# Optimization experiments

Measured on AMD Instinct MI355X. Metric: run time of the kernel, lower is better.

Reference implementation:

```python
import jax, jax.numpy as jnp
import numpy as np

B, N_HEADS, DIM, Z, X = 128, 12, 768, 7, 14


def _rpe_index(z, x):
    """2D concatenated self-attention relative positional encoding index.
    Tokens = z*z template tokens followed by x*x search tokens. Two token
    pairs share a bias index iff they have the same (dh, dw, region_i, region_j).
    """
    zh, zw = np.meshgrid(np.arange(z), np.arange(z), indexing='ij')
    xh, xw = np.meshgrid(np.arange(x), np.arange(x), indexing='ij')
    h = np.concatenate([zh.ravel(), xh.ravel()])
    w = np.concatenate([zw.ravel(), xw.ravel()])
    region = np.concatenate([np.zeros(z * z, np.int64), np.ones(x * x, np.int64)])
    dh = h[:, None] - h[None, :]
    dw = w[:, None] - w[None, :]
    rb = np.broadcast_to(region[:, None], dh.shape)
    rc = np.broadcast_to(region[None, :], dh.shape)
    key = np.stack([dh, dw, rb, rc], axis=-1).reshape(-1, 4)
    _, inv = np.unique(key, axis=0, return_inverse=True)
    return inv.reshape(dh.shape)  # (N, N) int


def setup_inputs() -> dict:
    key = jax.random.key(0)
    ks = jax.random.split(key, 4)
    N = Z * Z + X * X  # 245
    idx = _rpe_index(Z, X)
    n_bias = int(idx.max()) + 1
    return {
        "x": jax.random.normal(ks[0], (B, N, DIM), jnp.float32),
        "qkv_w": jax.random.normal(ks[1], (3 * DIM, DIM), jnp.float32) * 0.02,
        "proj_w": jax.random.normal(ks[2], (DIM, DIM), jnp.float32) * 0.02,
        "proj_b": jnp.zeros((DIM,), jnp.float32),
        "bias_table": jax.random.normal(ks[3], (N_HEADS, n_bias), jnp.float32) * 0.02,
        "rel_index": jnp.asarray(idx, jnp.int32),
    }


def reference(x, qkv_w, proj_w, proj_b, bias_table, rel_index):
    Bq, N, C = x.shape
    H = N_HEADS
    Dh = C // H
    scale = Dh ** -0.5
    # qkv projection (no bias): (B, N, 3, H, Dh)
    qkv = (x @ qkv_w.T).reshape(Bq, N, 3, H, Dh)
    q = jnp.moveaxis(qkv[:, :, 0], 2, 1)  # (B, H, N, Dh)
    k = jnp.moveaxis(qkv[:, :, 1], 2, 1)
    v = jnp.moveaxis(qkv[:, :, 2], 2, 1)
    attn = jnp.einsum('bhnd,bhmd->bhnm', q, k) * scale  # (B, H, N, N)
    # relative position bias gather: (H, N, N) broadcast over batch
    attn = attn + bias_table[:, rel_index][None]
    attn = jax.nn.softmax(attn, axis=-1)
    out = jnp.einsum('bhnm,bhmd->bhnd', attn, v)  # (B, H, N, Dh)
    out = jnp.moveaxis(out, 1, 2).reshape(Bq, N, C)
    return out @ proj_w.T + proj_b
```

## Files before the change

### kernel.cpp

```cpp
#include <hip/hip_runtime.h>
#include <hip/hip_bf16.h>
#include <stdint.h>
#include <math.h>

#define BATCH 128
#define NTOK 245
#define HEADS 12
#define DHEAD 64
#define CDIM 768
#define KT 24
#define SUBT 512
#define SCL 0.18033688f
#define PCLAMP 43.3f

typedef __attribute__((ext_vector_type(8))) short short8;
typedef __attribute__((ext_vector_type(4))) float f32x4;

__device__ __forceinline__ float bf2f(uint32_t hbits) {
    union { uint32_t u; float f; } v; v.u = hbits << 16; return v.f;
}
__device__ __forceinline__ uint32_t f2bf(float f) {
    union { float f; uint32_t u; } v; v.f = f;
    return (v.u + 0x7fffu + ((v.u >> 16) & 1u)) >> 16;
}
__device__ __forceinline__ ushort2 pk2bf(float x, float y) {
    union { __hip_bfloat162 h; ushort2 u; } c;
    c.h = __float22bfloat162_rn(make_float2(x, y));
    return c.u;
}
__device__ __forceinline__ size_t tiled_addr(int m, int k) {
    return (((size_t)(m >> 4) * KT + (k >> 5)) * 64 + ((k >> 3) & 3) * 16 + (m & 15)) * 8
           + (k & 7);
}
__device__ __forceinline__ void gl_lds16(const uint16_t* g, ushort* lds) {
    __builtin_amdgcn_global_load_lds(
        (const __attribute__((address_space(1))) void*)g,
        (__attribute__((address_space(3))) void*)lds,
        16, 0, 0);
}

#define N8_X  3010560
#define N8_WQ  221184
#define N8_WP   73728
__global__ __launch_bounds__(256)
void cvt_all(const float* __restrict__ x, const float* __restrict__ wq,
             const float* __restrict__ wp, uint16_t* __restrict__ xd,
             uint16_t* __restrict__ wqd, uint16_t* __restrict__ wpd)
{
    int i = blockIdx.x * 256 + threadIdx.x;
    const int stride = gridDim.x * 256;
    const int total = N8_X + N8_WQ + N8_WP;
    for (; i < total; i += stride) {
        const float* src; uint16_t* dst; int j;
        if (i < N8_X)              { src = x;  dst = xd;  j = i; }
        else if (i < N8_X + N8_WQ) { src = wq; dst = wqd; j = i - N8_X; }
        else                       { src = wp; dst = wpd; j = i - N8_X - N8_WQ; }
        const int sl = j & 63;
        const int tile = j >> 6;
        const int rt = tile / KT, kt = tile - rt * KT;
        const size_t soff = (size_t)(rt * 16 + (sl & 15)) * CDIM + kt * 32 + (sl >> 4) * 8;
        float4 a = *(const float4*)(src + soff);
        float4 b = *(const float4*)(src + soff + 4);
        ushort2 p0 = pk2bf(a.x, a.y), p1 = pk2bf(a.z, a.w);
        ushort2 p2 = pk2bf(b.x, b.y), p3 = pk2bf(b.z, b.w);
        uint4 o;
        o.x = (uint32_t)p0.x | ((uint32_t)p0.y << 16);
        o.y = (uint32_t)p1.x | ((uint32_t)p1.y << 16);
        o.z = (uint32_t)p2.x | ((uint32_t)p2.y << 16);
        o.w = (uint32_t)p3.x | ((uint32_t)p3.y << 16);
        *(uint4*)(dst + (size_t)j * 8) = o;
    }
}

__global__ __launch_bounds__(256)
void bias_pre(const float* __restrict__ bias_table, const int* __restrict__ rel,
              int n_bias, uint16_t* __restrict__ bias_t)
{
    const int h = blockIdx.x, j = blockIdx.y, q = threadIdx.x;
    float v = -43281.f;
    if (j < NTOK && q < NTOK)
        v = bias_table[(size_t)h * n_bias + rel[q * NTOK + j]] * 1.44269504f;
    bias_t[((size_t)h * 256 + j) * 256 + q] = (uint16_t)f2bf(v);
}

#define GEMM_LOOP                                                                \
    gl_lds16(gA0, &Af[0][w  ][0][0]);                                            \
    gl_lds16(gA1, &Af[0][w+4][0][0]);                                            \
    gl_lds16(gB0, &Bf[0][w  ][0][0]);                                            \
    gl_lds16(gB1, &Bf[0][w+4][0][0]);                                            \
    gl_lds16(gA0 + SUBT, &Af[1][w  ][0][0]);                                     \
    gl_lds16(gA1 + SUBT, &Af[1][w+4][0][0]);                                     \
    gl_lds16(gB0 + SUBT, &Bf[1][w  ][0][0]);                                     \
    gl_lds16(gB1 + SUBT, &Bf[1][w+4][0][0]);                                     \
    int cur = 0, nxt = 2;                                                        \
    _Pragma("unroll 1")                                                          \
    for (int t = 0; t < KT; ++t) {                                               \
        if (t == KT - 1) { asm volatile("s_waitcnt vmcnt(0) lgkmcnt(0)" ::: "memory"); } \
        else             { asm volatile("s_waitcnt vmcnt(4) lgkmcnt(0)" ::: "memory"); } \
        __builtin_amdgcn_s_barrier();                                            \
        if (t + 2 < KT) {                                                        \
            const int ko = (t + 2) * SUBT;                                       \
            gl_lds16(gA0 + ko, &Af[nxt][w  ][0][0]);                             \
            gl_lds16(gA1 + ko, &Af[nxt][w+4][0][0]);                             \
            gl_lds16(gB0 + ko, &Bf[nxt][w  ][0][0]);                             \
            gl_lds16(gB1 + ko, &Bf[nxt][w+4][0][0]);                             \
        }                                                                        \
        short8 af[4], bf[4];                                                     \
        _Pragma("unroll")                                                        \
        for (int m = 0; m < 4; ++m)                                              \
            af[m] = *(const short8*)&Af[cur][wr*4 + m][l][0];                    \
        _Pragma("unroll")                                                        \
        for (int n = 0; n < 4; ++n)                                              \
            bf[n] = *(const short8*)&Bf[cur][wc*4 + n][l][0];                    \
        _Pragma("unroll")                                                        \
        for (int m = 0; m < 4; ++m)                                              \
            _Pragma("unroll")                                                    \
            for (int n = 0; n < 4; ++n)                                          \
                acc[m][n] = __builtin_amdgcn_mfma_f32_16x16x32_bf16(bf[n], af[m], acc[m][n], 0, 0, 0); \
        cur = (cur == 2) ? 0 : cur + 1;                                          \
        nxt = (nxt == 2) ? 0 : nxt + 1;                                          \
    }

__global__ __launch_bounds__(256)
void qkv_gemm_mfma(const uint16_t* __restrict__ xb, const uint16_t* __restrict__ wq,
                   uint16_t* __restrict__ qkv)
{
    __shared__ ushort Af[3][8][64][8];
    __shared__ ushort Bf[3][8][64][8];
    const int t = threadIdx.x;
    const int w = t >> 6, l = t & 63;
    const int wr = w >> 1, wc = w & 1;
    const int lm = l & 15, lk = l >> 4;

    const int bid = blockIdx.x;
    const int xcd = bid & 7;
    const int wg = (xcd < 2 ? xcd * 552 : 1104 + (xcd - 2) * 551) + (bid >> 3);
    const int mtile = wg / 18, ctile = wg - mtile * 18;
    const int m0 = mtile * 128, c0 = ctile * 128;

    const uint16_t* gA0 = xb + ((size_t)(mtile*8 + w    ) * KT * 64 + l) * 8;
    const uint16_t* gA1 = xb + ((size_t)(mtile*8 + w + 4) * KT * 64 + l) * 8;
    const uint16_t* gB0 = wq + ((size_t)(ctile*8 + w    ) * KT * 64 + l) * 8;
    const uint16_t* gB1 = wq + ((size_t)(ctile*8 + w + 4) * KT * 64 + l) * 8;

    f32x4 acc[4][4];
    #pragma unroll
    for (int m = 0; m < 4; ++m)
        #pragma unroll
        for (int n = 0; n < 4; ++n) acc[m][n] = (f32x4){0.f,0.f,0.f,0.f};

    GEMM_LOOP

    int sArr[4], hArr[4], dArr[4];
    #pragma unroll
    for (int n = 0; n < 4; ++n) {
        int c = c0 + wc*64 + n*16 + lk*4;
        int s = c / CDIM; int rem = c - s * CDIM;
        sArr[n] = s; hArr[n] = rem >> 6; dArr[n] = rem & 63;
    }
    #pragma unroll
    for (int m = 0; m < 4; ++m) {
        int gm  = m0 + wr*64 + m*16 + lm;
        int b   = gm / NTOK;
        int tok = gm - b * NTOK;
        #pragma unroll
        for (int n = 0; n < 4; ++n) {
            ushort2 u0 = pk2bf(acc[m][n][0], acc[m][n][1]);
            ushort2 u1 = pk2bf(acc[m][n][2], acc[m][n][3]);
            uint2 pk;
            pk.x = (uint32_t)u0.x | ((uint32_t)u0.y << 16);
            pk.y = (uint32_t)u1.x | ((uint32_t)u1.y << 16);
            size_t addr = ((((size_t)b*3 + sArr[n])*HEADS + hArr[n])*NTOK + tok)*DHEAD + dArr[n];
            *(uint2*)(qkv + addr) = pk;
        }
    }
}

__global__ __launch_bounds__(512)
void attn_mfma(const uint16_t* __restrict__ qkv, const uint16_t* __restrict__ bias_t,
               uint16_t* __restrict__ o_t)
{
    __shared__ ushort Ks[256][72];
    __shared__ ushort Vt[64][264];
    __shared__ ushort Ps[8][16][72];
    const int bh = blockIdx.x;
    const int b = bh / HEADS, h = bh % HEADS;
    const int t = threadIdx.x;
    const int w = t >> 6, l = t & 63;
    const int lm = l & 15, lk = l >> 4;
    const int wq0 = w * 32;

    const uint16_t* qbase = qkv + (((size_t)b*3 + 0)*HEADS + h) * (NTOK*DHEAD);
    const uint16_t* kbase = qkv + (((size_t)b*3 + 1)*HEADS + h) * (NTOK*DHEAD);
    const uint16_t* vbase = qkv + (((size_t)b*3 + 2)*HEADS + h) * (NTOK*DHEAD);
    const uint16_t* btab  = bias_t + (size_t)h * 256 * 256;

    {
        const int col = (t & 7) * 8;
        #pragma unroll
        for (int p = 0; p < 4; ++p) {
            int row = p * 64 + (t >> 3);
            uint4 val = make_uint4(0u,0u,0u,0u);
            if (row < NTOK) val = *(const uint4*)(kbase + (size_t)row * DHEAD + col);
            *(uint4*)&Ks[row][col] = val;
        }
    }
    {
        const int j  = t >> 1;
        const int dh = (t & 1) * 32;
        uint4 r0 = make_uint4(0,0,0,0), r1 = r0, r2 = r0, r3 = r0;
        if (j < NTOK) {
            const uint16_t* src = vbase + (size_t)j * DHEAD + dh;
            r0 = *(const uint4*)(src);
            r1 = *(const uint4*)(src + 8);
            r2 = *(const uint4*)(src + 16);
            r3 = *(const uint4*)(src + 24);
        }
        union { uint4 v[4]; ushort s[32]; } u;
        u.v[0] = r0; u.v[1] = r1; u.v[2] = r2; u.v[3] = r3;
        #pragma unroll
        for (int i = 0; i < 32; ++i)
            Vt[dh + i][j] = u.s[i];
    }

    short8 qf[2][2];
    #pragma unroll
    for (int m = 0; m < 2; ++m) {
        int qrow = wq0 + m*16 + lm; if (qrow > NTOK-1) qrow = NTOK-1;
        #pragma unroll
        for (int k2 = 0; k2 < 2; ++k2)
            qf[m][k2] = *(const short8*)(qbase + (size_t)qrow * DHEAD + k2*32 + lk*8);
    }

    f32x4 acc_o[2][4];
    float lsum[2][4];
    #pragma unroll
    for (int m = 0; m < 2; ++m) {
        #pragma unroll
        for (int n = 0; n < 4; ++n) acc_o[m][n] = (f32x4){0.f,0.f,0.f,0.f};
        #pragma unroll
        for (int r = 0; r < 4; ++r) lsum[m][r] = 0.f;
    }

    __syncthreads();

    for (int jb = 0; jb < 4; ++jb) {
        short8 kf[4][2], vf[4][2];
        #pragma unroll
        for (int n = 0; n < 4; ++n)
            #pragma unroll
            for (int k2 = 0; k2 < 2; ++k2) {
                kf[n][k2] = *(const short8*)&Ks[jb*64 + n*16 + lm][k2*32 + lk*8];
                vf[n][k2] = *(const short8*)&Vt[n*16 + lm][jb*64 + k2*32 + lk*8];
            }

        #pragma unroll
        for (int m = 0; m < 2; ++m) {
            f32x4 sv[4];
            __builtin_amdgcn_s_setprio(1);
            #pragma unroll
            for (int n = 0; n < 4; ++n) {
                f32x4 z = (f32x4){0.f,0.f,0.f,0.f};
                sv[n] = __builtin_amdgcn_mfma_f32_16x16x32_bf16(qf[m][0], kf[n][0], z, 0, 0, 0);
                sv[n] = __builtin_amdgcn_mfma_f32_16x16x32_bf16(qf[m][1], kf[n][1], sv[n], 0, 0, 0);
            }
            __builtin_amdgcn_s_setprio(0);
            #pragma unroll
            for (int n = 0; n < 4; ++n) {
                uint2 bb = *(const uint2*)(btab + (size_t)(jb*64 + n*16 + lm) * 256 + wq0 + m*16 + lk*4);
                float s0 = fmaf(sv[n][0], SCL, bf2f(bb.x & 0xffffu));
                float s1 = fmaf(sv[n][1], SCL, bf2f(bb.x >> 16));
                float s2 = fmaf(sv[n][2], SCL, bf2f(bb.y & 0xffffu));
                float s3 = fmaf(sv[n][3], SCL, bf2f(bb.y >> 16));
                sv[n][0] = exp2f(fminf(s0, PCLAMP));
                sv[n][1] = exp2f(fminf(s1, PCLAMP));
                sv[n][2] = exp2f(fminf(s2, PCLAMP));
                sv[n][3] = exp2f(fminf(s3, PCLAMP));
            }
            #pragma unroll
            for (int n = 0; n < 4; ++n)
                #pragma unroll
                for (int r = 0; r < 4; ++r) {
                    ushort u = pk2bf(sv[n][r], sv[n][r]).x;
                    lsum[m][r] += bf2f(u);
                    Ps[w][lk*4 + r][n*16 + lm] = u;
                }
            short8 pf[2];
            #pragma unroll
            for (int k2 = 0; k2 < 2; ++k2)
                pf[k2] = *(const short8*)&Ps[w][lm][k2*32 + lk*8];
            __builtin_amdgcn_s_setprio(1);
            #pragma unroll
            for (int n = 0; n < 4; ++n) {
                acc_o[m][n] = __builtin_amdgcn_mfma_f32_16x16x32_bf16(pf[0], vf[n][0], acc_o[m][n], 0, 0, 0);
                acc_o[m][n] = __builtin_amdgcn_mfma_f32_16x16x32_bf16(pf[1], vf[n][1], acc_o[m][n], 0, 0, 0);
            }
            __builtin_amdgcn_s_setprio(0);
        }
    }

    #pragma unroll
    for (int m = 0; m < 2; ++m) {
        float inv[4];
        #pragma unroll
        for (int r = 0; r < 4; ++r) {
            float s = lsum[m][r];
            s += __shfl_xor(s, 1);
            s += __shfl_xor(s, 2);
            s += __shfl_xor(s, 4);
            s += __shfl_xor(s, 8);
            inv[r] = 1.f / s;
        }
        #pragma unroll
        for (int r = 0; r < 4; ++r) {
            int q = wq0 + m*16 + lk*4 + r;
            if (q < NTOK) {
                int gm = b * NTOK + q;
                #pragma unroll
                for (int n = 0; n < 4; ++n) {
                    int k = h * DHEAD + n*16 + lm;
                    o_t[tiled_addr(gm, k)] = (uint16_t)f2bf(acc_o[m][n][r] * inv[r]);
                }
            }
        }
    }
}

__global__ __launch_bounds__(256)
void proj_gemm_mfma(const uint16_t* __restrict__ ot, const uint16_t* __restrict__ wp,
                    const float* __restrict__ bias, float* __restrict__ out)
{
    __shared__ ushort Af[3][8][64][8];
    __shared__ ushort Bf[3][8][64][8];
    const int t = threadIdx.x;
    const int w = t >> 6, l = t & 63;
    const int wr = w >> 1, wc = w & 1;
    const int lm = l & 15, lk = l >> 4;

    const int bid = blockIdx.x;
    const int xcd = bid & 7;
    const int wg = (xcd < 6 ? xcd * 184 : 1104 + (xcd - 6) * 183) + (bid >> 3);
    const int mtile = wg / 6, ctile = wg - mtile * 6;
    const int m0 = mtile * 128, c0 = ctile * 128;

    const uint16_t* gA0 = ot + ((size_t)(mtile*8 + w    ) * KT * 64 + l) * 8;
    const uint16_t* gA1 = ot + ((size_t)(mtile*8 + w + 4) * KT * 64 + l) * 8;
    const uint16_t* gB0 = wp + ((size_t)(ctile*8 + w    ) * KT * 64 + l) * 8;
    const uint16_t* gB1 = wp + ((size_t)(ctile*8 + w + 4) * KT * 64 + l) * 8;

    f32x4 acc[4][4];
    #pragma unroll
    for (int m = 0; m < 4; ++m)
        #pragma unroll
        for (int n = 0; n < 4; ++n) acc[m][n] = (f32x4){0.f,0.f,0.f,0.f};

    GEMM_LOOP

    float4 bsv[4]; int cArr[4];
    #pragma unroll
    for (int n = 0; n < 4; ++n) {
        cArr[n] = c0 + wc*64 + n*16 + lk*4;
        bsv[n]  = *(const float4*)(bias + cArr[n]);
    }
    #pragma unroll
    for (int m = 0; m < 4; ++m) {
        int gm = m0 + wr*64 + m*16 + lm;
        #pragma unroll
        for (int n = 0; n < 4; ++n) {
            float4 r;
            r.x = acc[m][n][0] + bsv[n].x;
            r.y = acc[m][n][1] + bsv[n].y;
            r.z = acc[m][n][2] + bsv[n].z;
            r.w = acc[m][n][3] + bsv[n].w;
            *(float4*)(out + (size_t)gm * CDIM + cArr[n]) = r;
        }
    }
}

extern "C" void kernel_launch(void* const* d_in, const int* in_sizes, int n_in,
                              void* d_out, int out_size, void* d_ws, size_t ws_size,
                              hipStream_t stream)
{
    (void)n_in; (void)out_size;
    const float* x          = (const float*)d_in[0];
    const float* qkv_w      = (const float*)d_in[1];
    const float* proj_w     = (const float*)d_in[2];
    const float* proj_b     = (const float*)d_in[3];
    const float* bias_table = (const float*)d_in[4];
    const int*   rel        = (const int*)d_in[5];
    const int n_bias = in_sizes[4] / HEADS;

    const size_t qkv_elems = (size_t)BATCH * 3 * HEADS * NTOK * DHEAD;
    const size_t o_elems   = (size_t)BATCH * HEADS * NTOK * DHEAD;
    const size_t bt_elems  = (size_t)HEADS * 256 * 256;
    const size_t wq_elems  = (size_t)3 * CDIM * CDIM;
    const size_t wp_elems  = (size_t)CDIM * CDIM;

    uint16_t* qkv_ws = (uint16_t*)d_ws;
    uint16_t* o_ws   = qkv_ws + qkv_elems;
    uint16_t* bt_ws  = o_ws + o_elems;
    uint16_t* wq_ws  = bt_ws + bt_elems;
    uint16_t* wp_ws  = wq_ws + wq_elems;
    const size_t need = (qkv_elems + o_elems + bt_elems + wq_elems + wp_elems) * sizeof(uint16_t);
    if (ws_size < need) return;

    uint16_t* xb = o_ws;

    cvt_all<<<2048, 256, 0, stream>>>(x, qkv_w, proj_w, xb, wq_ws, wp_ws);

    bias_pre<<<dim3(HEADS, 256), 256, 0, stream>>>(bias_table, rel, n_bias, bt_ws);

    qkv_gemm_mfma<<<4410, 256, 0, stream>>>(xb, wq_ws, qkv_ws);

    attn_mfma<<<dim3(BATCH * HEADS), 512, 0, stream>>>(qkv_ws, bt_ws, o_ws);

    proj_gemm_mfma<<<1470, 256, 0, stream>>>(o_ws, wp_ws, proj_b, (float*)d_out);
}
```

Baseline: 321.6 us.

## Load GEMM B operand directly from global into registers, dropping its LDS staging

In both the QKV and projection GEMMs, the weight (B) tiles are no longer staged through shared memory. Each wave loads its four B fragments straight from global memory into registers, one k-step ahead, while only A stays triple-buffered in LDS. This halves LDS footprint and LDS read traffic, and cuts the async copies per k-step. In exchange, every wave pair sharing a column block fetches the same B data twice from global/L2. The register-prefetch latency must also be hidden by the adjusted vmcnt wait, which may stall if the loads are slow.

```diff
diff --git a/kernel.cpp b/kernel.cpp
--- a/kernel.cpp
+++ b/kernel.cpp
@@ -10,6 +10,7 @@
 #define CDIM 768
 #define KT 24
 #define SUBT 512
+#define BSTR (KT*64*8)
 #define SCL 0.18033688f
 #define PCLAMP 43.3f
 
@@ -83,40 +84,46 @@
     bias_t[((size_t)h * 256 + j) * 256 + q] = (uint16_t)f2bf(v);
 }
 
-#define GEMM_LOOP                                                                \
-    gl_lds16(gA0, &Af[0][w  ][0][0]);                                            \
-    gl_lds16(gA1, &Af[0][w+4][0][0]);                                            \
-    gl_lds16(gB0, &Bf[0][w  ][0][0]);                                            \
-    gl_lds16(gB1, &Bf[0][w+4][0][0]);                                            \
+#define GEMM_LOOP_BDIR                                                           \
+    gl_lds16(gA0,        &Af[0][w  ][0][0]);                                     \
+    gl_lds16(gA1,        &Af[0][w+4][0][0]);                                     \
     gl_lds16(gA0 + SUBT, &Af[1][w  ][0][0]);                                     \
     gl_lds16(gA1 + SUBT, &Af[1][w+4][0][0]);                                     \
-    gl_lds16(gB0 + SUBT, &Bf[1][w  ][0][0]);                                     \
-    gl_lds16(gB1 + SUBT, &Bf[1][w+4][0][0]);                                     \
+    short8 bc0 = *(const short8*)(gB);                                           \
+    short8 bc1 = *(const short8*)(gB + BSTR);                                    \
+    short8 bc2 = *(const short8*)(gB + 2*BSTR);                                  \
+    short8 bc3 = *(const short8*)(gB + 3*BSTR);                                  \
+    short8 bn0, bn1, bn2, bn3;                                                   \
     int cur = 0, nxt = 2;                                                        \
     _Pragma("unroll 1")                                                          \
     for (int t = 0; t < KT; ++t) {                                               \
         if (t == KT - 1) { asm volatile("s_waitcnt vmcnt(0) lgkmcnt(0)" ::: "memory"); } \
-        else             { asm volatile("s_waitcnt vmcnt(4) lgkmcnt(0)" ::: "memory"); } \
+        else             { asm volatile("s_waitcnt vmcnt(6) lgkmcnt(0)" ::: "memory"); } \
         __builtin_amdgcn_s_barrier();                                            \
         if (t + 2 < KT) {                                                        \
             const int ko = (t + 2) * SUBT;                                       \
             gl_lds16(gA0 + ko, &Af[nxt][w  ][0][0]);                             \
             gl_lds16(gA1 + ko, &Af[nxt][w+4][0][0]);                             \
-            gl_lds16(gB0 + ko, &Bf[nxt][w  ][0][0]);                             \
-            gl_lds16(gB1 + ko, &Bf[nxt][w+4][0][0]);                             \
         }                                                                        \
-        short8 af[4], bf[4];                                                     \
+        if (t + 1 < KT) {                                                        \
+            const uint16_t* gbn = gB + (t + 1) * SUBT;                           \
+            bn0 = *(const short8*)(gbn);                                         \
+            bn1 = *(const short8*)(gbn + BSTR);                                  \
+            bn2 = *(const short8*)(gbn + 2*BSTR);                                \
+            bn3 = *(const short8*)(gbn + 3*BSTR);                                \
+        }                                                                        \
+        short8 af[4];                                                            \
         _Pragma("unroll")                                                        \
         for (int m = 0; m < 4; ++m)                                              \
             af[m] = *(const short8*)&Af[cur][wr*4 + m][l][0];                    \
         _Pragma("unroll")                                                        \
-        for (int n = 0; n < 4; ++n)                                              \
-            bf[n] = *(const short8*)&Bf[cur][wc*4 + n][l][0];                    \
-        _Pragma("unroll")                                                        \
-        for (int m = 0; m < 4; ++m)                                              \
-            _Pragma("unroll")                                                    \
-            for (int n = 0; n < 4; ++n)                                          \
-                acc[m][n] = __builtin_amdgcn_mfma_f32_16x16x32_bf16(bf[n], af[m], acc[m][n], 0, 0, 0); \
+        for (int m = 0; m < 4; ++m) {                                            \
+            acc[m][0] = __builtin_amdgcn_mfma_f32_16x16x32_bf16(bc0, af[m], acc[m][0], 0, 0, 0); \
+            acc[m][1] = __builtin_amdgcn_mfma_f32_16x16x32_bf16(bc1, af[m], acc[m][1], 0, 0, 0); \
+            acc[m][2] = __builtin_amdgcn_mfma_f32_16x16x32_bf16(bc2, af[m], acc[m][2], 0, 0, 0); \
+            acc[m][3] = __builtin_amdgcn_mfma_f32_16x16x32_bf16(bc3, af[m], acc[m][3], 0, 0, 0); \
+        }                                                                        \
+        if (t + 1 < KT) { bc0 = bn0; bc1 = bn1; bc2 = bn2; bc3 = bn3; }          \
         cur = (cur == 2) ? 0 : cur + 1;                                          \
         nxt = (nxt == 2) ? 0 : nxt + 1;                                          \
     }
@@ -126,7 +133,6 @@
                    uint16_t* __restrict__ qkv)
 {
     __shared__ ushort Af[3][8][64][8];
-    __shared__ ushort Bf[3][8][64][8];
     const int t = threadIdx.x;
     const int w = t >> 6, l = t & 63;
     const int wr = w >> 1, wc = w & 1;
@@ -140,8 +146,7 @@
 
     const uint16_t* gA0 = xb + ((size_t)(mtile*8 + w    ) * KT * 64 + l) * 8;
     const uint16_t* gA1 = xb + ((size_t)(mtile*8 + w + 4) * KT * 64 + l) * 8;
-    const uint16_t* gB0 = wq + ((size_t)(ctile*8 + w    ) * KT * 64 + l) * 8;
-    const uint16_t* gB1 = wq + ((size_t)(ctile*8 + w + 4) * KT * 64 + l) * 8;
+    const uint16_t* gB  = wq + ((size_t)(ctile*8 + wc*4) * KT * 64 + l) * 8;
 
     f32x4 acc[4][4];
     #pragma unroll
@@ -149,7 +154,7 @@
         #pragma unroll
         for (int n = 0; n < 4; ++n) acc[m][n] = (f32x4){0.f,0.f,0.f,0.f};
 
-    GEMM_LOOP
+    GEMM_LOOP_BDIR
 
     int sArr[4], hArr[4], dArr[4];
     #pragma unroll
@@ -331,7 +336,6 @@
                     const float* __restrict__ bias, float* __restrict__ out)
 {
     __shared__ ushort Af[3][8][64][8];
-    __shared__ ushort Bf[3][8][64][8];
     const int t = threadIdx.x;
     const int w = t >> 6, l = t & 63;
     const int wr = w >> 1, wc = w & 1;
@@ -345,8 +349,7 @@
 
     const uint16_t* gA0 = ot + ((size_t)(mtile*8 + w    ) * KT * 64 + l) * 8;
     const uint16_t* gA1 = ot + ((size_t)(mtile*8 + w + 4) * KT * 64 + l) * 8;
-    const uint16_t* gB0 = wp + ((size_t)(ctile*8 + w    ) * KT * 64 + l) * 8;
-    const uint16_t* gB1 = wp + ((size_t)(ctile*8 + w + 4) * KT * 64 + l) * 8;
+    const uint16_t* gB  = wp + ((size_t)(ctile*8 + wc*4) * KT * 64 + l) * 8;
 
     f32x4 acc[4][4];
     #pragma unroll
@@ -354,7 +357,7 @@
         #pragma unroll
         for (int n = 0; n < 4; ++n) acc[m][n] = (f32x4){0.f,0.f,0.f,0.f};
 
-    GEMM_LOOP
+    GEMM_LOOP_BDIR
 
     float4 bsv[4]; int cArr[4];
     #pragma unroll
```

New measurement: 331.5 us. +3.1%, slower.
